# Kernel tuning notes

Measured on AMD Instinct MI355X. Metric: run time of the kernel, lower is better.

Reference implementation:

```python
import jax, jax.numpy as jnp
import numpy as np

# MoE config (matches init_kwargs)
T = 16384   # tokens
H = 1024    # hidden size
I = 1024    # intermediate size per expert
E = 8       # n_experts
TOPK = 2
RENORMALIZE = True


def setup_inputs() -> dict:
    key = jax.random.key(0)
    ks = jax.random.split(key, 6)
    x = jax.random.normal(ks[0], (T, H), dtype=jnp.float32)
    gating_output = jax.random.normal(ks[1], (T, E), dtype=jnp.float32)
    # fp8-quantized weights simulated as their integer-grid values in fp32;
    # dequant = q * per-expert scalar scale (normalize_e4m3fn_to_native_float8 path)
    w1 = jax.random.normal(ks[2], (E, 2 * I, H), dtype=jnp.float32)  # fused [gate; up]
    w2 = jax.random.normal(ks[3], (E, H, I), dtype=jnp.float32)      # down_proj
    w1_scale = jax.random.uniform(ks[4], (E,), dtype=jnp.float32, minval=0.01, maxval=0.05)
    w2_scale = jax.random.uniform(ks[5], (E,), dtype=jnp.float32, minval=0.01, maxval=0.05)
    return {"x": x, "gating_output": gating_output, "w1": w1, "w2": w2,
            "w1_scale": w1_scale, "w2_scale": w2_scale}


def _moe(x, gating_output, w1, w2, w1_scale, w2_scale):
    # softmax scoring -> top-k routing (use_grouped_topk=False)
    probs = jax.nn.softmax(gating_output, axis=-1)              # [T, E]
    topk_w, topk_idx = jax.lax.top_k(probs, TOPK)               # [T, K]
    if RENORMALIZE:
        topk_w = topk_w / jnp.sum(topk_w, axis=-1, keepdims=True)
    out = jnp.zeros_like(x)
    for e in range(E):  # fixed small expert count: grouped-GEMM reference
        w1e = w1[e] * w1_scale[e]                               # dequant [2I, H]
        w2e = w2[e] * w2_scale[e]                               # dequant [H, I]
        gate = x @ w1e[:I].T                                    # [T, I]
        up = x @ w1e[I:].T                                      # [T, I]
        h = jax.nn.silu(gate) * up                              # SwiGLU
        y = h @ w2e.T                                           # [T, H]
        # per-token routing weight for this expert (0 if not routed)
        coef = jnp.sum(jnp.where(topk_idx == e, topk_w, 0.0), axis=-1)  # [T]
        out = out + coef[:, None] * y
    return out


def reference(x, gating_output, w1, w2, w1_scale, w2_scale):
    return _moe(x, gating_output, w1, w2, w1_scale, w2_scale)
```

## Files before the change

### kernel.cpp

```cpp
#include <hip/hip_runtime.h>
#include <hip/hip_bf16.h>

#define T_TOK 16384
#define H_DIM 1024
#define I_DIM 1024
#define E_NUM 8
#define NPAIR (T_TOK * 2)
#define BM 128
#define BK 64
#define MAX_MT (NPAIR / BM + E_NUM)

typedef float v4f __attribute__((ext_vector_type(4)));
typedef float v16f __attribute__((ext_vector_type(16)));
typedef short v8s __attribute__((ext_vector_type(8)));

__device__ __forceinline__ unsigned short f2bf(float f) {
    unsigned int u = __float_as_uint(f);
    unsigned int r = (u + 0x7fffu + ((u >> 16) & 1u)) >> 16;
    return (unsigned short)r;
}
__device__ __forceinline__ float bf2f(unsigned short s) {
    return __uint_as_float(((unsigned int)s) << 16);
}

__device__ __forceinline__ void gl_lds16(const void* g, void* l) {
    __builtin_amdgcn_global_load_lds(
        (const __attribute__((address_space(1))) void*)g,
        (__attribute__((address_space(3))) void*)l, 16, 0, 0);
}

__device__ __forceinline__ int swz(int row, int unit) {
    return row * 64 + ((unit ^ (row & 7)) << 3);
}

__global__ void k_route(const float* __restrict__ gating,
                        int* __restrict__ tokExp, float* __restrict__ tokW,
                        int* __restrict__ counts) {
    int t = blockIdx.x * 256 + threadIdx.x;
    int lane = threadIdx.x & 63;
    float g[E_NUM];
#pragma unroll
    for (int e = 0; e < E_NUM; e++) g[e] = gating[t * E_NUM + e];
    int i0 = 0; float v0 = g[0];
#pragma unroll
    for (int e = 1; e < E_NUM; e++) if (g[e] > v0) { v0 = g[e]; i0 = e; }
    int i1 = -1; float v1 = -1e30f;
#pragma unroll
    for (int e = 0; e < E_NUM; e++) if (e != i0 && g[e] > v1) { v1 = g[e]; i1 = e; }
    float w0 = 1.f / (1.f + __expf(v1 - v0));
    tokExp[2 * t] = i0; tokExp[2 * t + 1] = i1;
    tokW[2 * t] = w0;   tokW[2 * t + 1] = 1.f - w0;
#pragma unroll
    for (int e = 0; e < E_NUM; e++) {
        unsigned long long mA = __ballot(i0 == e);
        unsigned long long mB = __ballot(i1 == e);
        int c = __popcll(mA) + __popcll(mB);
        if (lane == 0 && c) atomicAdd(&counts[e], c);
    }
}

__global__ void k_scan(const int* __restrict__ counts, int* __restrict__ offsets,
                       int* __restrict__ tileOff, int* __restrict__ cursor) {
    if (threadIdx.x == 0 && blockIdx.x == 0) {
        int o = 0, to = 0;
        for (int e = 0; e < E_NUM; e++) {
            offsets[e] = o; tileOff[e] = to; cursor[e] = o;
            o += counts[e]; to += (counts[e] + BM - 1) / BM;
        }
        offsets[E_NUM] = o; tileOff[E_NUM] = to;
    }
}

__global__ void k_scatter(const int* __restrict__ tokExp, const float* __restrict__ tokW,
                          int* __restrict__ cursor,
                          int* __restrict__ pairTok, float* __restrict__ pairW,
                          int* __restrict__ invMap) {
    int t = blockIdx.x * 256 + threadIdx.x;
    int lane = threadIdx.x & 63;
#pragma unroll
    for (int k = 0; k < 2; k++) {
        int e = tokExp[2 * t + k];
        int pos = 0;
#pragma unroll
        for (int ex = 0; ex < E_NUM; ex++) {
            unsigned long long m = __ballot(e == ex);
            if (m) {
                int leader = __builtin_ctzll(m);
                int base = 0;
                if (lane == leader) base = atomicAdd(&cursor[ex], __popcll(m));
                base = __shfl(base, leader);
                if (e == ex) pos = base + __popcll(m & ((1ull << lane) - 1ull));
            }
        }
        pairTok[pos] = t;
        pairW[pos] = tokW[2 * t + k];
        invMap[2 * t + k] = pos;
    }
}

__global__ void k_cvt_x(const float* __restrict__ src, unsigned short* __restrict__ dst) {
    size_t i4 = ((size_t)blockIdx.x * 256 + threadIdx.x) * 4;
    float4 v = *(const float4*)(src + i4);
    ushort4 o;
    o.x = f2bf(v.x); o.y = f2bf(v.y); o.z = f2bf(v.z); o.w = f2bf(v.w);
    *(ushort4*)(dst + i4) = o;
}

__global__ void k_cvt_w(const float* __restrict__ src, unsigned short* __restrict__ dst,
                        const float* __restrict__ scale, int shift) {
    size_t i4 = ((size_t)blockIdx.x * 256 + threadIdx.x) * 4;
    float s = scale[i4 >> shift];
    float4 v = *(const float4*)(src + i4);
    ushort4 o;
    o.x = f2bf(v.x * s); o.y = f2bf(v.y * s); o.z = f2bf(v.z * s); o.w = f2bf(v.w * s);
    *(ushort4*)(dst + i4) = o;
}

__global__ __launch_bounds__(256, 2)
void k_gemm1(const unsigned short* __restrict__ xbf,
             const unsigned short* __restrict__ w1bf,
             const int* __restrict__ pairTok,
             const int* __restrict__ offsets, const int* __restrict__ tileOff,
             unsigned short* __restrict__ hbuf) {
    __shared__ unsigned short lA[BM * BK];
    __shared__ unsigned short lB[256 * BK];

    int mt = blockIdx.x;
    if (mt >= tileOff[E_NUM]) return;
    int e = 0;
    while (mt >= tileOff[e + 1]) e++;
    int row0 = offsets[e] + (mt - tileOff[e]) * BM;
    int valid = offsets[e + 1] - row0; if (valid > BM) valid = BM;

    int nt = blockIdx.y;
    int tid = threadIdx.x;
    int lane = tid & 63, wave = tid >> 6;
    int wm = wave >> 1, wn = wave & 1;

    int lr = lane >> 3;
    int lcs = ((lane & 7) ^ lr) * 8;

    const unsigned short* wg = w1bf + (size_t)e * 2 * I_DIM * H_DIM + (size_t)(nt * 128) * H_DIM;
    const unsigned short* wu = wg + (size_t)I_DIM * H_DIM;
    const unsigned short* bsrc = (wave & 2) ? wu : wg;
    int brow0 = (wave & 1) * 64;

    int tokRow[4];
#pragma unroll
    for (int j = 0; j < 4; j++) {
        int r = wave * 32 + j * 8 + lr;
        int rc = r < valid ? r : valid - 1;
        tokRow[j] = pairTok[row0 + rc];
    }

    v16f ag[2][2], au[2][2];
#pragma unroll
    for (int i = 0; i < 2; i++)
#pragma unroll
        for (int j = 0; j < 2; j++) { ag[i][j] = (v16f)0.f; au[i][j] = (v16f)0.f; }

    for (int ko = 0; ko < H_DIM / BK; ko++) {
        int k0 = ko * BK;
        __syncthreads();
#pragma unroll
        for (int j = 0; j < 4; j++)
            gl_lds16(xbf + (size_t)tokRow[j] * H_DIM + k0 + lcs, lA + (wave * 4 + j) * 512);
#pragma unroll
        for (int j = 0; j < 8; j++)
            gl_lds16(bsrc + (size_t)(brow0 + j * 8 + lr) * H_DIM + k0 + lcs,
                     lB + (wave * 8 + j) * 512);
        __syncthreads();
#pragma unroll
        for (int kk = 0; kk < BK; kk += 16) {
            int u = (kk >> 3) + (lane >> 5);
            v8s a[2], bg[2], bu[2];
#pragma unroll
            for (int i = 0; i < 2; i++)
                a[i] = *(const v8s*)(lA + swz(wm * 64 + i * 32 + (lane & 31), u));
#pragma unroll
            for (int j = 0; j < 2; j++) {
                int rb = wn * 64 + j * 32 + (lane & 31);
                bg[j] = *(const v8s*)(lB + swz(rb, u));
                bu[j] = *(const v8s*)(lB + swz(128 + rb, u));
            }
#pragma unroll
            for (int i = 0; i < 2; i++)
#pragma unroll
                for (int j = 0; j < 2; j++) {
                    ag[i][j] = __builtin_amdgcn_mfma_f32_32x32x16_bf16(a[i], bg[j], ag[i][j], 0, 0, 0);
                    au[i][j] = __builtin_amdgcn_mfma_f32_32x32x16_bf16(a[i], bu[j], au[i][j], 0, 0, 0);
                }
        }
    }

    int half = lane >> 5, c = lane & 31;
#pragma unroll
    for (int i = 0; i < 2; i++)
#pragma unroll
        for (int r = 0; r < 16; r++) {
            int row = wm * 64 + i * 32 + (r & 3) + 8 * (r >> 2) + 4 * half;
            if (row < valid) {
                size_t base = (size_t)(row0 + row) * I_DIM + nt * 128 + wn * 64;
#pragma unroll
                for (int j = 0; j < 2; j++) {
                    float g = ag[i][j][r];
                    float uu = au[i][j][r];
                    float s = g / (1.f + __expf(-g));
                    hbuf[base + j * 32 + c] = f2bf(s * uu);
                }
            }
        }
}

__global__ __launch_bounds__(256, 2)
void k_gemm2(const unsigned short* __restrict__ hbuf,
             const unsigned short* __restrict__ w2bf,
             const float* __restrict__ pairW,
             const int* __restrict__ offsets, const int* __restrict__ tileOff,
             unsigned short* __restrict__ ybuf) {
    __shared__ unsigned short lA[BM * BK];
    __shared__ unsigned short lB[256 * BK];

    int mt = blockIdx.x;
    if (mt >= tileOff[E_NUM]) return;
    int e = 0;
    while (mt >= tileOff[e + 1]) e++;
    int row0 = offsets[e] + (mt - tileOff[e]) * BM;
    int valid = offsets[e + 1] - row0; if (valid > BM) valid = BM;

    int nt = blockIdx.y;
    int tid = threadIdx.x;
    int lane = tid & 63, wave = tid >> 6;
    int wm = wave >> 1, wn = wave & 1;

    int lr = lane >> 3;
    int lcs = ((lane & 7) ^ lr) * 8;

    const unsigned short* w2e = w2bf + (size_t)e * H_DIM * I_DIM + (size_t)(nt * 256) * I_DIM;

    int rowA[4];
#pragma unroll
    for (int j = 0; j < 4; j++) {
        int r = wave * 32 + j * 8 + lr;
        int rc = r < valid ? r : valid - 1;
        rowA[j] = row0 + rc;
    }

    v16f acc[2][4];
#pragma unroll
    for (int i = 0; i < 2; i++)
#pragma unroll
        for (int j = 0; j < 4; j++) acc[i][j] = (v16f)0.f;

    for (int ko = 0; ko < I_DIM / BK; ko++) {
        int k0 = ko * BK;
        __syncthreads();
#pragma unroll
        for (int j = 0; j < 4; j++)
            gl_lds16(hbuf + (size_t)rowA[j] * I_DIM + k0 + lcs, lA + (wave * 4 + j) * 512);
#pragma unroll
        for (int j = 0; j < 8; j++)
            gl_lds16(w2e + (size_t)(wave * 64 + j * 8 + lr) * I_DIM + k0 + lcs,
                     lB + (wave * 8 + j) * 512);
        __syncthreads();
#pragma unroll
        for (int kk = 0; kk < BK; kk += 16) {
            int u = (kk >> 3) + (lane >> 5);
            v8s a[2], b[4];
#pragma unroll
            for (int i = 0; i < 2; i++)
                a[i] = *(const v8s*)(lA + swz(wm * 64 + i * 32 + (lane & 31), u));
#pragma unroll
            for (int j = 0; j < 4; j++)
                b[j] = *(const v8s*)(lB + swz(wn * 128 + j * 32 + (lane & 31), u));
#pragma unroll
            for (int i = 0; i < 2; i++)
#pragma unroll
                for (int j = 0; j < 4; j++)
                    acc[i][j] = __builtin_amdgcn_mfma_f32_32x32x16_bf16(a[i], b[j], acc[i][j], 0, 0, 0);
        }
    }

    int half = lane >> 5, c = lane & 31;
#pragma unroll
    for (int i = 0; i < 2; i++)
#pragma unroll
        for (int r = 0; r < 16; r++) {
            int row = wm * 64 + i * 32 + (r & 3) + 8 * (r >> 2) + 4 * half;
            if (row < valid) {
                int pos = row0 + row;
                float coef = pairW[pos];
                unsigned short* orow = ybuf + (size_t)pos * H_DIM + nt * 256 + wn * 128;
#pragma unroll
                for (int j = 0; j < 4; j++)
                    orow[j * 32 + c] = f2bf(coef * acc[i][j][r]);
            }
        }
}

__global__ __launch_bounds__(256)
void k_reduce(const unsigned short* __restrict__ ybuf,
              const int* __restrict__ invMap,
              float* __restrict__ out) {
    int t = blockIdx.x;
    int p0 = invMap[2 * t], p1 = invMap[2 * t + 1];
    int c4 = threadIdx.x * 4;
    ushort4 a = *(const ushort4*)(ybuf + (size_t)p0 * H_DIM + c4);
    ushort4 b = *(const ushort4*)(ybuf + (size_t)p1 * H_DIM + c4);
    float4 o;
    o.x = bf2f(a.x) + bf2f(b.x);
    o.y = bf2f(a.y) + bf2f(b.y);
    o.z = bf2f(a.z) + bf2f(b.z);
    o.w = bf2f(a.w) + bf2f(b.w);
    *(float4*)(out + (size_t)t * H_DIM + c4) = o;
}

extern "C" void kernel_launch(void* const* d_in, const int* in_sizes, int n_in,
                              void* d_out, int out_size, void* d_ws, size_t ws_size,
                              hipStream_t stream) {
    const float* x      = (const float*)d_in[0];
    const float* gating = (const float*)d_in[1];
    const float* w1     = (const float*)d_in[2];
    const float* w2     = (const float*)d_in[3];
    const float* w1s    = (const float*)d_in[4];
    const float* w2s    = (const float*)d_in[5];
    float* out = (float*)d_out;

    char* ws = (char*)d_ws;
    size_t off = 0;
    auto alloc = [&](size_t bytes) { void* p = ws + off; off += (bytes + 255) & ~(size_t)255; return p; };
    unsigned short* xbf  = (unsigned short*)alloc((size_t)T_TOK * H_DIM * 2);
    unsigned short* w1bf = (unsigned short*)alloc((size_t)E_NUM * 2 * I_DIM * H_DIM * 2);
    unsigned short* w2bf = (unsigned short*)alloc((size_t)E_NUM * H_DIM * I_DIM * 2);
    unsigned short* hbuf = (unsigned short*)alloc((size_t)NPAIR * I_DIM * 2);
    unsigned short* ybuf = (unsigned short*)alloc((size_t)NPAIR * H_DIM * 2);
    int*   pairTok = (int*)alloc(NPAIR * 4);
    float* pairW   = (float*)alloc(NPAIR * 4);
    int*   tokExp  = (int*)alloc(NPAIR * 4);
    float* tokW    = (float*)alloc(NPAIR * 4);
    int*   invMap  = (int*)alloc(NPAIR * 4);
    int*   counts  = (int*)alloc(64);
    int*   offsets = (int*)alloc(64);
    int*   tileOff = (int*)alloc(64);
    int*   cursor  = (int*)alloc(64);

    hipMemsetAsync(counts, 0, 64, stream);

    k_route<<<T_TOK / 256, 256, 0, stream>>>(gating, tokExp, tokW, counts);
    k_scan<<<1, 64, 0, stream>>>(counts, offsets, tileOff, cursor);
    k_scatter<<<T_TOK / 256, 256, 0, stream>>>(tokExp, tokW, cursor, pairTok, pairW, invMap);
    k_cvt_x<<<(T_TOK * H_DIM / 4) / 256, 256, 0, stream>>>(x, xbf);
    k_cvt_w<<<(E_NUM * 2 * I_DIM * H_DIM / 4) / 256, 256, 0, stream>>>(w1, w1bf, w1s, 21);
    k_cvt_w<<<(E_NUM * H_DIM * I_DIM / 4) / 256, 256, 0, stream>>>(w2, w2bf, w2s, 20);

    dim3 g1(MAX_MT, I_DIM / 128);
    k_gemm1<<<g1, 256, 0, stream>>>(xbf, w1bf, pairTok, offsets, tileOff, hbuf);
    dim3 g2(MAX_MT, H_DIM / 256);
    k_gemm2<<<g2, 256, 0, stream>>>(hbuf, w2bf, pairW, offsets, tileOff, ybuf);
    k_reduce<<<T_TOK, 256, 0, stream>>>(ybuf, invMap, out);
}
```

Measured before the change: 569.9 us.

## Shrink GEMM tiles and split gate/up accumulation across waves for higher occupancy

GEMM1 now computes 64 intermediate columns per block. Half the waves accumulate the gate projection and half the up projection, and the up results are passed to the gate waves through LDS (rounded to bf16) before the SwiGLU epilogue. GEMM2 uses 64-row M tiles with a separate tile offset table. Both kernels raise the launch-bounds occupancy target from 2 to 3. The aim is to cut accumulator register pressure and raise occupancy and block count. The cost is lower per-block data reuse, more global traffic for x and h, an extra LDS round trip with bf16 rounding of the up values, and idle waves during the epilogue.

```diff
diff --git a/kernel.cpp b/kernel.cpp
--- a/kernel.cpp
+++ b/kernel.cpp
@@ -7,8 +7,10 @@
 #define E_NUM 8
 #define NPAIR (T_TOK * 2)
 #define BM 128
+#define BM2 64
 #define BK 64
 #define MAX_MT (NPAIR / BM + E_NUM)
+#define MAX_MT2 (NPAIR / BM2 + E_NUM)
 
 typedef float v4f __attribute__((ext_vector_type(4)));
 typedef float v16f __attribute__((ext_vector_type(16)));
@@ -60,14 +62,17 @@
 }
 
 __global__ void k_scan(const int* __restrict__ counts, int* __restrict__ offsets,
-                       int* __restrict__ tileOff, int* __restrict__ cursor) {
+                       int* __restrict__ tileOff, int* __restrict__ tileOff2,
+                       int* __restrict__ cursor) {
     if (threadIdx.x == 0 && blockIdx.x == 0) {
-        int o = 0, to = 0;
+        int o = 0, to = 0, to2 = 0;
         for (int e = 0; e < E_NUM; e++) {
-            offsets[e] = o; tileOff[e] = to; cursor[e] = o;
-            o += counts[e]; to += (counts[e] + BM - 1) / BM;
-        }
-        offsets[E_NUM] = o; tileOff[E_NUM] = to;
+            offsets[e] = o; tileOff[e] = to; tileOff2[e] = to2; cursor[e] = o;
+            o += counts[e];
+            to += (counts[e] + BM - 1) / BM;
+            to2 += (counts[e] + BM2 - 1) / BM2;
+        }
+        offsets[E_NUM] = o; tileOff[E_NUM] = to; tileOff2[E_NUM] = to2;
     }
 }
 
@@ -116,14 +121,14 @@
     *(ushort4*)(dst + i4) = o;
 }
 
-__global__ __launch_bounds__(256, 2)
+__global__ __launch_bounds__(256, 3)
 void k_gemm1(const unsigned short* __restrict__ xbf,
              const unsigned short* __restrict__ w1bf,
              const int* __restrict__ pairTok,
              const int* __restrict__ offsets, const int* __restrict__ tileOff,
              unsigned short* __restrict__ hbuf) {
     __shared__ unsigned short lA[BM * BK];
-    __shared__ unsigned short lB[256 * BK];
+    __shared__ unsigned short lB[BM * BK];
 
     int mt = blockIdx.x;
     if (mt >= tileOff[E_NUM]) return;
@@ -135,15 +140,14 @@
     int nt = blockIdx.y;
     int tid = threadIdx.x;
     int lane = tid & 63, wave = tid >> 6;
-    int wm = wave >> 1, wn = wave & 1;
+    int wm = wave & 1, role = wave >> 1;
 
     int lr = lane >> 3;
     int lcs = ((lane & 7) ^ lr) * 8;
 
-    const unsigned short* wg = w1bf + (size_t)e * 2 * I_DIM * H_DIM + (size_t)(nt * 128) * H_DIM;
+    const unsigned short* wg = w1bf + (size_t)e * 2 * I_DIM * H_DIM + (size_t)(nt * 64) * H_DIM;
     const unsigned short* wu = wg + (size_t)I_DIM * H_DIM;
     const unsigned short* bsrc = (wave & 2) ? wu : wg;
-    int brow0 = (wave & 1) * 64;
 
     int tokRow[4];
 #pragma unroll
@@ -153,11 +157,11 @@
         tokRow[j] = pairTok[row0 + rc];
     }
 
-    v16f ag[2][2], au[2][2];
+    v16f acc[2][2];
 #pragma unroll
     for (int i = 0; i < 2; i++)
 #pragma unroll
-        for (int j = 0; j < 2; j++) { ag[i][j] = (v16f)0.f; au[i][j] = (v16f)0.f; }
+        for (int j = 0; j < 2; j++) acc[i][j] = (v16f)0.f;
 
     for (int ko = 0; ko < H_DIM / BK; ko++) {
         int k0 = ko * BK;
@@ -166,98 +170,107 @@
         for (int j = 0; j < 4; j++)
             gl_lds16(xbf + (size_t)tokRow[j] * H_DIM + k0 + lcs, lA + (wave * 4 + j) * 512);
 #pragma unroll
-        for (int j = 0; j < 8; j++)
-            gl_lds16(bsrc + (size_t)(brow0 + j * 8 + lr) * H_DIM + k0 + lcs,
-                     lB + (wave * 8 + j) * 512);
+        for (int j = 0; j < 4; j++) {
+            int srcrow = (wave & 1) * 32 + j * 8 + lr;
+            gl_lds16(bsrc + (size_t)srcrow * H_DIM + k0 + lcs, lB + (wave * 4 + j) * 512);
+        }
         __syncthreads();
 #pragma unroll
         for (int kk = 0; kk < BK; kk += 16) {
             int u = (kk >> 3) + (lane >> 5);
-            v8s a[2], bg[2], bu[2];
+            v8s a[2], b[2];
 #pragma unroll
             for (int i = 0; i < 2; i++)
                 a[i] = *(const v8s*)(lA + swz(wm * 64 + i * 32 + (lane & 31), u));
 #pragma unroll
-            for (int j = 0; j < 2; j++) {
-                int rb = wn * 64 + j * 32 + (lane & 31);
-                bg[j] = *(const v8s*)(lB + swz(rb, u));
-                bu[j] = *(const v8s*)(lB + swz(128 + rb, u));
+            for (int j = 0; j < 2; j++)
+                b[j] = *(const v8s*)(lB + swz(role * 64 + j * 32 + (lane & 31), u));
+#pragma unroll
+            for (int i = 0; i < 2; i++)
+#pragma unroll
+                for (int j = 0; j < 2; j++)
+                    acc[i][j] = __builtin_amdgcn_mfma_f32_32x32x16_bf16(a[i], b[j], acc[i][j], 0, 0, 0);
+        }
+    }
+
+    int half = lane >> 5, c = lane & 31;
+    __syncthreads();
+    if (role == 1) {
+#pragma unroll
+        for (int i = 0; i < 2; i++)
+#pragma unroll
+            for (int r = 0; r < 16; r++) {
+                int row = wm * 64 + i * 32 + (r & 3) + 8 * (r >> 2) + 4 * half;
+#pragma unroll
+                for (int j = 0; j < 2; j++)
+                    lB[row * 64 + j * 32 + c] = f2bf(acc[i][j][r]);
             }
-#pragma unroll
-            for (int i = 0; i < 2; i++)
-#pragma unroll
-                for (int j = 0; j < 2; j++) {
-                    ag[i][j] = __builtin_amdgcn_mfma_f32_32x32x16_bf16(a[i], bg[j], ag[i][j], 0, 0, 0);
-                    au[i][j] = __builtin_amdgcn_mfma_f32_32x32x16_bf16(a[i], bu[j], au[i][j], 0, 0, 0);
-                }
-        }
-    }
-
-    int half = lane >> 5, c = lane & 31;
-#pragma unroll
-    for (int i = 0; i < 2; i++)
-#pragma unroll
-        for (int r = 0; r < 16; r++) {
-            int row = wm * 64 + i * 32 + (r & 3) + 8 * (r >> 2) + 4 * half;
-            if (row < valid) {
-                size_t base = (size_t)(row0 + row) * I_DIM + nt * 128 + wn * 64;
-#pragma unroll
-                for (int j = 0; j < 2; j++) {
-                    float g = ag[i][j][r];
-                    float uu = au[i][j][r];
-                    float s = g / (1.f + __expf(-g));
-                    hbuf[base + j * 32 + c] = f2bf(s * uu);
+    }
+    __syncthreads();
+    if (role == 0) {
+#pragma unroll
+        for (int i = 0; i < 2; i++)
+#pragma unroll
+            for (int r = 0; r < 16; r++) {
+                int row = wm * 64 + i * 32 + (r & 3) + 8 * (r >> 2) + 4 * half;
+                if (row < valid) {
+                    size_t base = (size_t)(row0 + row) * I_DIM + nt * 64;
+#pragma unroll
+                    for (int j = 0; j < 2; j++) {
+                        float g = acc[i][j][r];
+                        float uu = bf2f(lB[row * 64 + j * 32 + c]);
+                        float s = g / (1.f + __expf(-g));
+                        hbuf[base + j * 32 + c] = f2bf(s * uu);
+                    }
                 }
             }
-        }
-}
-
-__global__ __launch_bounds__(256, 2)
+    }
+}
+
+__global__ __launch_bounds__(256, 3)
 void k_gemm2(const unsigned short* __restrict__ hbuf,
              const unsigned short* __restrict__ w2bf,
              const float* __restrict__ pairW,
-             const int* __restrict__ offsets, const int* __restrict__ tileOff,
+             const int* __restrict__ offsets, const int* __restrict__ tileOff2,
              unsigned short* __restrict__ ybuf) {
-    __shared__ unsigned short lA[BM * BK];
+    __shared__ unsigned short lA[BM2 * BK];
     __shared__ unsigned short lB[256 * BK];
 
     int mt = blockIdx.x;
-    if (mt >= tileOff[E_NUM]) return;
+    if (mt >= tileOff2[E_NUM]) return;
     int e = 0;
-    while (mt >= tileOff[e + 1]) e++;
-    int row0 = offsets[e] + (mt - tileOff[e]) * BM;
-    int valid = offsets[e + 1] - row0; if (valid > BM) valid = BM;
+    while (mt >= tileOff2[e + 1]) e++;
+    int row0 = offsets[e] + (mt - tileOff2[e]) * BM2;
+    int valid = offsets[e + 1] - row0; if (valid > BM2) valid = BM2;
 
     int nt = blockIdx.y;
     int tid = threadIdx.x;
     int lane = tid & 63, wave = tid >> 6;
-    int wm = wave >> 1, wn = wave & 1;
+    int wm = wave & 1, wn = wave >> 1;
 
     int lr = lane >> 3;
     int lcs = ((lane & 7) ^ lr) * 8;
 
     const unsigned short* w2e = w2bf + (size_t)e * H_DIM * I_DIM + (size_t)(nt * 256) * I_DIM;
 
-    int rowA[4];
-#pragma unroll
-    for (int j = 0; j < 4; j++) {
-        int r = wave * 32 + j * 8 + lr;
+    int rowA[2];
+#pragma unroll
+    for (int j = 0; j < 2; j++) {
+        int r = wave * 16 + j * 8 + lr;
         int rc = r < valid ? r : valid - 1;
         rowA[j] = row0 + rc;
     }
 
-    v16f acc[2][4];
-#pragma unroll
-    for (int i = 0; i < 2; i++)
-#pragma unroll
-        for (int j = 0; j < 4; j++) acc[i][j] = (v16f)0.f;
+    v16f acc[4];
+#pragma unroll
+    for (int j = 0; j < 4; j++) acc[j] = (v16f)0.f;
 
     for (int ko = 0; ko < I_DIM / BK; ko++) {
         int k0 = ko * BK;
         __syncthreads();
 #pragma unroll
-        for (int j = 0; j < 4; j++)
-            gl_lds16(hbuf + (size_t)rowA[j] * I_DIM + k0 + lcs, lA + (wave * 4 + j) * 512);
+        for (int j = 0; j < 2; j++)
+            gl_lds16(hbuf + (size_t)rowA[j] * I_DIM + k0 + lcs, lA + (wave * 2 + j) * 512);
 #pragma unroll
         for (int j = 0; j < 8; j++)
             gl_lds16(w2e + (size_t)(wave * 64 + j * 8 + lr) * I_DIM + k0 + lcs,
@@ -266,36 +279,30 @@
 #pragma unroll
         for (int kk = 0; kk < BK; kk += 16) {
             int u = (kk >> 3) + (lane >> 5);
-            v8s a[2], b[4];
-#pragma unroll
-            for (int i = 0; i < 2; i++)
-                a[i] = *(const v8s*)(lA + swz(wm * 64 + i * 32 + (lane & 31), u));
+            v8s a = *(const v8s*)(lA + swz(wm * 32 + (lane & 31), u));
+            v8s b[4];
 #pragma unroll
             for (int j = 0; j < 4; j++)
                 b[j] = *(const v8s*)(lB + swz(wn * 128 + j * 32 + (lane & 31), u));
 #pragma unroll
-            for (int i = 0; i < 2; i++)
-#pragma unroll
-                for (int j = 0; j < 4; j++)
-                    acc[i][j] = __builtin_amdgcn_mfma_f32_32x32x16_bf16(a[i], b[j], acc[i][j], 0, 0, 0);
+            for (int j = 0; j < 4; j++)
+                acc[j] = __builtin_amdgcn_mfma_f32_32x32x16_bf16(a, b[j], acc[j], 0, 0, 0);
         }
     }
 
     int half = lane >> 5, c = lane & 31;
 #pragma unroll
-    for (int i = 0; i < 2; i++)
-#pragma unroll
-        for (int r = 0; r < 16; r++) {
-            int row = wm * 64 + i * 32 + (r & 3) + 8 * (r >> 2) + 4 * half;
-            if (row < valid) {
-                int pos = row0 + row;
-                float coef = pairW[pos];
-                unsigned short* orow = ybuf + (size_t)pos * H_DIM + nt * 256 + wn * 128;
-#pragma unroll
-                for (int j = 0; j < 4; j++)
-                    orow[j * 32 + c] = f2bf(coef * acc[i][j][r]);
-            }
-        }
+    for (int r = 0; r < 16; r++) {
+        int row = wm * 32 + (r & 3) + 8 * (r >> 2) + 4 * half;
+        if (row < valid) {
+            int pos = row0 + row;
+            float coef = pairW[pos];
+            unsigned short* orow = ybuf + (size_t)pos * H_DIM + nt * 256 + wn * 128;
+#pragma unroll
+            for (int j = 0; j < 4; j++)
+                orow[j * 32 + c] = f2bf(coef * acc[j][r]);
+        }
+    }
 }
 
 __global__ __launch_bounds__(256)
@@ -334,28 +341,29 @@
     unsigned short* w2bf = (unsigned short*)alloc((size_t)E_NUM * H_DIM * I_DIM * 2);
     unsigned short* hbuf = (unsigned short*)alloc((size_t)NPAIR * I_DIM * 2);
     unsigned short* ybuf = (unsigned short*)alloc((size_t)NPAIR * H_DIM * 2);
-    int*   pairTok = (int*)alloc(NPAIR * 4);
-    float* pairW   = (float*)alloc(NPAIR * 4);
-    int*   tokExp  = (int*)alloc(NPAIR * 4);
-    float* tokW    = (float*)alloc(NPAIR * 4);
-    int*   invMap  = (int*)alloc(NPAIR * 4);
-    int*   counts  = (int*)alloc(64);
-    int*   offsets = (int*)alloc(64);
-    int*   tileOff = (int*)alloc(64);
-    int*   cursor  = (int*)alloc(64);
+    int*   pairTok  = (int*)alloc(NPAIR * 4);
+    float* pairW    = (float*)alloc(NPAIR * 4);
+    int*   tokExp   = (int*)alloc(NPAIR * 4);
+    float* tokW     = (float*)alloc(NPAIR * 4);
+    int*   invMap   = (int*)alloc(NPAIR * 4);
+    int*   counts   = (int*)alloc(64);
+    int*   offsets  = (int*)alloc(64);
+    int*   tileOff  = (int*)alloc(64);
+    int*   tileOff2 = (int*)alloc(64);
+    int*   cursor   = (int*)alloc(64);
 
     hipMemsetAsync(counts, 0, 64, stream);
 
     k_route<<<T_TOK / 256, 256, 0, stream>>>(gating, tokExp, tokW, counts);
-    k_scan<<<1, 64, 0, stream>>>(counts, offsets, tileOff, cursor);
+    k_scan<<<1, 64, 0, stream>>>(counts, offsets, tileOff, tileOff2, cursor);
     k_scatter<<<T_TOK / 256, 256, 0, stream>>>(tokExp, tokW, cursor, pairTok, pairW, invMap);
     k_cvt_x<<<(T_TOK * H_DIM / 4) / 256, 256, 0, stream>>>(x, xbf);
     k_cvt_w<<<(E_NUM * 2 * I_DIM * H_DIM / 4) / 256, 256, 0, stream>>>(w1, w1bf, w1s, 21);
     k_cvt_w<<<(E_NUM * H_DIM * I_DIM / 4) / 256, 256, 0, stream>>>(w2, w2bf, w2s, 20);
 
-    dim3 g1(MAX_MT, I_DIM / 128);
+    dim3 g1(MAX_MT, I_DIM / 64);
     k_gemm1<<<g1, 256, 0, stream>>>(xbf, w1bf, pairTok, offsets, tileOff, hbuf);
-    dim3 g2(MAX_MT, H_DIM / 256);
-    k_gemm2<<<g2, 256, 0, stream>>>(hbuf, w2bf, pairW, offsets, tileOff, ybuf);
+    dim3 g2(MAX_MT2, H_DIM / 256);
+    k_gemm2<<<g2, 256, 0, stream>>>(hbuf, w2bf, pairW, offsets, tileOff2, ybuf);
     k_reduce<<<T_TOK, 256, 0, stream>>>(ybuf, invMap, out);
 }
```

Result: no change. 580.6 us (+1.9%).
